# Kernel tuning notes

Hardware: AMD Instinct MI355X
Metric: run time of the kernel (lower is better)

The kernel has to match this reference:

```python
import jax, jax.numpy as jnp
import numpy as np

P, Q = 3, 3          # degrees
M, N = 127, 127      # max span index per direction (ctrl grid is (M+1)x(N+1))
DIM = 3
SU, SV = 256, 256    # out_dim_u, out_dim_v
B = 16
EPS = 1e-08


def _normalize_knots(knots):
    # cumsum of positive increments, rescaled to [0, 1]
    kc = jnp.cumsum(jnp.where(knots < 0.0, 0.0001, knots), axis=1)
    return (kc - kc[:, :1]) / (kc[:, -1:] - kc[:, :1])


def _find_spans(t, K, deg, max_span):
    # t: [S], K: [B, LK] -> spans [B, S] (first interior knot with t - K > EPS, else 1 sentinel)
    d = t[None, None, :] - K[:, deg:-deg, None]          # [B, L_int, S]
    masked = jnp.where(d > EPS, d, 1.0)
    return jnp.clip(jnp.argmin(masked, axis=1) + deg, deg, max_span)


def _basis(t, K, span, deg):
    # Cox-de Boor recursion. t: [S], K: [B, LK], span: [B, S] int -> [B, deg+1, S]
    Bsz, S = span.shape
    tb = t[None, :]
    Ni = [jnp.zeros((Bsz, S), K.dtype) for _ in range(deg + 1)]
    Ni[0] = jnp.ones((Bsz, S), K.dtype)
    for k in range(1, deg + 1):
        saved = jnp.zeros((Bsz, S), K.dtype)
        for r in range(k):
            K1 = jnp.take_along_axis(K, span + r + 1, axis=1)       # [B, S]
            K2 = jnp.take_along_axis(K, span + 1 - k + r, axis=1)   # [B, S]
            denom = (K1 - tb) + (tb - K2)
            temp = jnp.where(denom == 0.0, 0.0001,
                             Ni[r] / jnp.where(denom == 0.0, 1.0, denom))
            Ni[r] = saved + (K1 - tb) * temp
            saved = (tb - K2) * temp
        Ni[k] = saved
    return jnp.stack(Ni, axis=1)


def setup_inputs() -> dict:
    key = jax.random.key(0)
    k1, k2, k3 = jax.random.split(key, 3)
    ctrl_pts = jax.random.normal(k1, (B, M + 1, N + 1, DIM), dtype=jnp.float32)
    knot_u = jax.random.uniform(k2, (B, M + P + 2), dtype=jnp.float32)
    knot_v = jax.random.uniform(k3, (B, N + Q + 2), dtype=jnp.float32)
    u = jnp.linspace(1e-05, 1.0 - 1e-05, SU, dtype=jnp.float32)
    v = jnp.linspace(1e-05, 1.0 - 1e-05, SV, dtype=jnp.float32)
    return {"ctrl_pts": ctrl_pts, "knot_u": knot_u, "knot_v": knot_v, "u": u, "v": v}


def reference(ctrl_pts, knot_u, knot_v, u, v):
    U = _normalize_knots(knot_u)   # [B, M+P+2]
    V = _normalize_knots(knot_v)
    uspan = _find_spans(u, U, P, M)   # [B, SU] int
    vspan = _find_spans(v, V, Q, N)   # [B, SV] int
    Nu = _basis(u, U, uspan, P)       # [B, P+1, SU]
    Nv = _basis(v, V, vspan, Q)       # [B, Q+1, SV]
    # gather control points: pts[b,l,r,i,j,:] = ctrl_pts[b, uspan[b,i]-P+l, vspan[b,j]-Q+r, :]
    u_idx = uspan[:, None, :] - P + jnp.arange(P + 1)[None, :, None]  # [B, P+1, SU]
    v_idx = vspan[:, None, :] - Q + jnp.arange(Q + 1)[None, :, None]  # [B, Q+1, SV]
    b_idx = jnp.arange(B)[:, None, None, None, None]
    pts = ctrl_pts[b_idx,
                   u_idx[:, :, None, :, None],
                   v_idx[:, None, :, None, :], :]  # [B, P+1, Q+1, SU, SV, DIM]
    surfaces = jnp.einsum('bpquvd,bpu,bqv->buvd', pts, Nu, Nv)
    return surfaces[..., :DIM]
```

## Files before the change

kernel.cpp:

```cpp
#include <hip/hip_runtime.h>

#define BATCH 16
#define PDEG  3
#define MAXSPAN 127
#define KLEN  132
#define NSAMP 256
#define NSPANS 126
#define GRID_PTS 128
#define ROWF (GRID_PTS * 3)

__device__ __align__(16) float g_N[2][BATCH][NSAMP][4];
__device__ int   g_span[2][BATCH][NSAMP];

__global__ void basis_kernel(const float* __restrict__ knot_u,
                             const float* __restrict__ knot_v,
                             const float* __restrict__ u_arr,
                             const float* __restrict__ v_arr)
{
    __shared__ double sA[KLEN];
    __shared__ double sB[KLEN];
    const int b    = blockIdx.x;
    const int axis = blockIdx.y;
    const int tid  = threadIdx.x;

    const float* __restrict__ knots = axis ? knot_v : knot_u;
    const float* __restrict__ t_arr = axis ? v_arr  : u_arr;

    if (tid < KLEN) {
        float w = knots[b * KLEN + tid];
        sA[tid] = (w < 0.0f) ? 1.0e-4 : (double)w;
    }
    __syncthreads();

    double* src = sA;
    double* dst = sB;
    for (int off = 1; off < KLEN; off <<= 1) {
        if (tid < KLEN) {
            double v = src[tid];
            if (tid >= off) v += src[tid - off];
            dst[tid] = v;
        }
        __syncthreads();
        double* t_ = src; src = dst; dst = t_;
    }
    const double k0  = src[0];
    const double inv = 1.0 / (src[KLEN - 1] - k0);
    if (tid < KLEN) dst[tid] = (src[tid] - k0) * inv;
    __syncthreads();
    const double* __restrict__ kn = dst;

    const double t = (double)t_arr[tid];

    double best = 1.0e300;
    int jmin = 0;
    for (int j = 0; j < NSPANS; ++j) {
        double d = t - kn[j + PDEG];
        double m = (d > 1.0e-8) ? d : 1.0;
        if (m < best) { best = m; jmin = j; }
    }
    int span = jmin + PDEG;
    if (span > MAXSPAN) span = MAXSPAN;

    double Ni[PDEG + 1];
    Ni[0] = 1.0;
    for (int k = 1; k <= PDEG; ++k) {
        double saved = 0.0;
        for (int r = 0; r < k; ++r) {
            double K1 = kn[span + r + 1];
            double K2 = kn[span + 1 - k + r];
            double denom = (K1 - t) + (t - K2);
            double temp = (denom == 0.0) ? 1.0e-4 : (Ni[r] / denom);
            Ni[r] = saved + (K1 - t) * temp;
            saved = (t - K2) * temp;
        }
        Ni[k] = saved;
    }

    float4 o4;
    o4.x = (float)Ni[0]; o4.y = (float)Ni[1];
    o4.z = (float)Ni[2]; o4.w = (float)Ni[3];
    *(float4*)&g_N[axis][b][tid][0] = o4;
    g_span[axis][b][tid] = span;
}

__global__ void __launch_bounds__(256)
eval_kernel(const float* __restrict__ ctrl, float* __restrict__ out)
{
    __shared__ float s_tmp[ROWF];
    const int sv = threadIdx.x;
    const int su = blockIdx.x;
    const int b  = blockIdx.y;

    const int us = g_span[0][b][su];
    const float4 nu4 = *(const float4*)&g_N[0][b][su][0];

    const int vs = g_span[1][b][sv];
    const float4 nv4 = *(const float4*)&g_N[1][b][sv][0];
    const float nv[4] = {nv4.x, nv4.y, nv4.z, nv4.w};

    if (sv < ROWF / 4) {
        const float4* __restrict__ r0 = (const float4*)
            (ctrl + ((size_t)b * GRID_PTS + (size_t)(us - PDEG)) * ROWF);
        float4 a0 = r0[0 * 96 + sv];
        float4 a1 = r0[1 * 96 + sv];
        float4 a2 = r0[2 * 96 + sv];
        float4 a3 = r0[3 * 96 + sv];
        float4 t4;
        t4.x = nu4.x * a0.x + nu4.y * a1.x + nu4.z * a2.x + nu4.w * a3.x;
        t4.y = nu4.x * a0.y + nu4.y * a1.y + nu4.z * a2.y + nu4.w * a3.y;
        t4.z = nu4.x * a0.z + nu4.y * a1.z + nu4.z * a2.z + nu4.w * a3.z;
        t4.w = nu4.x * a0.w + nu4.y * a1.w + nu4.z * a2.w + nu4.w * a3.w;
        ((float4*)s_tmp)[sv] = t4;
    }

    __syncthreads();

    const float* tp = s_tmp + (vs - PDEG) * 3;
    float acc0 = 0.f, acc1 = 0.f, acc2 = 0.f;
#pragma unroll
    for (int q = 0; q < 4; ++q) {
        const float w = nv[q];
        acc0 += w * tp[q * 3 + 0];
        acc1 += w * tp[q * 3 + 1];
        acc2 += w * tp[q * 3 + 2];
    }

    const size_t o = (((size_t)b * NSAMP + su) * NSAMP + sv) * 3;
    out[o + 0] = acc0;
    out[o + 1] = acc1;
    out[o + 2] = acc2;
}

extern "C" void kernel_launch(void* const* d_in, const int* in_sizes, int n_in,
                              void* d_out, int out_size, void* d_ws, size_t ws_size,
                              hipStream_t stream) {
    const float* ctrl   = (const float*)d_in[0];
    const float* knot_u = (const float*)d_in[1];
    const float* knot_v = (const float*)d_in[2];
    const float* u      = (const float*)d_in[3];
    const float* v      = (const float*)d_in[4];
    float* out = (float*)d_out;

    dim3 bgrid(BATCH, 2);
    basis_kernel<<<bgrid, NSAMP, 0, stream>>>(knot_u, knot_v, u, v);

    dim3 egrid(NSAMP, BATCH);
    eval_kernel<<<egrid, NSAMP, 0, stream>>>(ctrl, out);
}
```

Measured before the change: 74.80 us.

## Fuse basis computation into surface evaluation kernel with per-block recompute

Merges the separate basis/span kernel into the evaluation kernel. Each block recomputes the normalized knots, the v basis for all samples and the u basis for its 16 rows in shared memory. It then processes 16 u-rows, two at a time, with double-buffered shared tmp rows. This removes a kernel launch and the global round-trip for basis data. In exchange the knot scan and span search are repeated redundantly per block, and the grid shrinks to 256 blocks, which may reduce parallelism.

```diff
diff --git a/kernel.cpp b/kernel.cpp
--- a/kernel.cpp
+++ b/kernel.cpp
@@ -8,49 +8,11 @@
 #define NSPANS 126
 #define GRID_PTS 128
 #define ROWF (GRID_PTS * 3)
+#define SU_PER_BLK 16
 
-__device__ __align__(16) float g_N[2][BATCH][NSAMP][4];
-__device__ int   g_span[2][BATCH][NSAMP];
-
-__global__ void basis_kernel(const float* __restrict__ knot_u,
-                             const float* __restrict__ knot_v,
-                             const float* __restrict__ u_arr,
-                             const float* __restrict__ v_arr)
+__device__ __forceinline__ int basis1(const double* __restrict__ kn,
+                                      double t, double Ni[PDEG + 1])
 {
-    __shared__ double sA[KLEN];
-    __shared__ double sB[KLEN];
-    const int b    = blockIdx.x;
-    const int axis = blockIdx.y;
-    const int tid  = threadIdx.x;
-
-    const float* __restrict__ knots = axis ? knot_v : knot_u;
-    const float* __restrict__ t_arr = axis ? v_arr  : u_arr;
-
-    if (tid < KLEN) {
-        float w = knots[b * KLEN + tid];
-        sA[tid] = (w < 0.0f) ? 1.0e-4 : (double)w;
-    }
-    __syncthreads();
-
-    double* src = sA;
-    double* dst = sB;
-    for (int off = 1; off < KLEN; off <<= 1) {
-        if (tid < KLEN) {
-            double v = src[tid];
-            if (tid >= off) v += src[tid - off];
-            dst[tid] = v;
-        }
-        __syncthreads();
-        double* t_ = src; src = dst; dst = t_;
-    }
-    const double k0  = src[0];
-    const double inv = 1.0 / (src[KLEN - 1] - k0);
-    if (tid < KLEN) dst[tid] = (src[tid] - k0) * inv;
-    __syncthreads();
-    const double* __restrict__ kn = dst;
-
-    const double t = (double)t_arr[tid];
-
     double best = 1.0e300;
     int jmin = 0;
     for (int j = 0; j < NSPANS; ++j) {
@@ -61,7 +23,6 @@
     int span = jmin + PDEG;
     if (span > MAXSPAN) span = MAXSPAN;
 
-    double Ni[PDEG + 1];
     Ni[0] = 1.0;
     for (int k = 1; k <= PDEG; ++k) {
         double saved = 0.0;
@@ -75,60 +36,133 @@
         }
         Ni[k] = saved;
     }
-
-    float4 o4;
-    o4.x = (float)Ni[0]; o4.y = (float)Ni[1];
-    o4.z = (float)Ni[2]; o4.w = (float)Ni[3];
-    *(float4*)&g_N[axis][b][tid][0] = o4;
-    g_span[axis][b][tid] = span;
+    return span;
 }
 
-__global__ void __launch_bounds__(256)
-eval_kernel(const float* __restrict__ ctrl, float* __restrict__ out)
+__global__ void __launch_bounds__(512)
+surf_kernel(const float* __restrict__ ctrl,
+            const float* __restrict__ knot_u,
+            const float* __restrict__ knot_v,
+            const float* __restrict__ u_arr,
+            const float* __restrict__ v_arr,
+            float* __restrict__ out)
 {
-    __shared__ float s_tmp[ROWF];
-    const int sv = threadIdx.x;
-    const int su = blockIdx.x;
-    const int b  = blockIdx.y;
+    __shared__ double sU[2][KLEN];
+    __shared__ double sV[2][KLEN];
+    __shared__ __align__(16) float sNv[NSAMP][4];
+    __shared__ int   sSv[NSAMP];
+    __shared__ __align__(16) float sNu[SU_PER_BLK][4];
+    __shared__ int   sSu[SU_PER_BLK];
+    __shared__ float s_tmp[2][2][ROWF];
 
-    const int us = g_span[0][b][su];
-    const float4 nu4 = *(const float4*)&g_N[0][b][su][0];
+    const int t   = threadIdx.x;
+    const int su0 = blockIdx.x * SU_PER_BLK;
+    const int b   = blockIdx.y;
 
-    const int vs = g_span[1][b][sv];
-    const float4 nv4 = *(const float4*)&g_N[1][b][sv][0];
-    const float nv[4] = {nv4.x, nv4.y, nv4.z, nv4.w};
-
-    if (sv < ROWF / 4) {
-        const float4* __restrict__ r0 = (const float4*)
-            (ctrl + ((size_t)b * GRID_PTS + (size_t)(us - PDEG)) * ROWF);
-        float4 a0 = r0[0 * 96 + sv];
-        float4 a1 = r0[1 * 96 + sv];
-        float4 a2 = r0[2 * 96 + sv];
-        float4 a3 = r0[3 * 96 + sv];
-        float4 t4;
-        t4.x = nu4.x * a0.x + nu4.y * a1.x + nu4.z * a2.x + nu4.w * a3.x;
-        t4.y = nu4.x * a0.y + nu4.y * a1.y + nu4.z * a2.y + nu4.w * a3.y;
-        t4.z = nu4.x * a0.z + nu4.y * a1.z + nu4.z * a2.z + nu4.w * a3.z;
-        t4.w = nu4.x * a0.w + nu4.y * a1.w + nu4.z * a2.w + nu4.w * a3.w;
-        ((float4*)s_tmp)[sv] = t4;
+    if (t < KLEN) {
+        float w = knot_u[b * KLEN + t];
+        sU[0][t] = (w < 0.0f) ? 1.0e-4 : (double)w;
+    } else if (t >= 256 && t < 256 + KLEN) {
+        const int i = t - 256;
+        float w = knot_v[b * KLEN + i];
+        sV[0][i] = (w < 0.0f) ? 1.0e-4 : (double)w;
     }
-
     __syncthreads();
 
-    const float* tp = s_tmp + (vs - PDEG) * 3;
-    float acc0 = 0.f, acc1 = 0.f, acc2 = 0.f;
+    int sb = 0;
+    for (int off = 1; off < KLEN; off <<= 1) {
+        if (t < KLEN) {
+            double v = sU[sb][t];
+            if (t >= off) v += sU[sb][t - off];
+            sU[sb ^ 1][t] = v;
+        } else if (t >= 256 && t < 256 + KLEN) {
+            const int i = t - 256;
+            double v = sV[sb][i];
+            if (i >= off) v += sV[sb][i - off];
+            sV[sb ^ 1][i] = v;
+        }
+        __syncthreads();
+        sb ^= 1;
+    }
+    if (t < KLEN) {
+        const double k0  = sU[sb][0];
+        const double inv = 1.0 / (sU[sb][KLEN - 1] - k0);
+        sU[sb ^ 1][t] = (sU[sb][t] - k0) * inv;
+    } else if (t >= 256 && t < 256 + KLEN) {
+        const int i = t - 256;
+        const double k0  = sV[sb][0];
+        const double inv = 1.0 / (sV[sb][KLEN - 1] - k0);
+        sV[sb ^ 1][i] = (sV[sb][i] - k0) * inv;
+    }
+    __syncthreads();
+    const double* __restrict__ knU = sU[sb ^ 1];
+    const double* __restrict__ knV = sV[sb ^ 1];
+
+    if (t < NSAMP) {
+        double Ni[PDEG + 1];
+        const int span = basis1(knV, (double)v_arr[t], Ni);
+        float4 o4;
+        o4.x = (float)Ni[0]; o4.y = (float)Ni[1];
+        o4.z = (float)Ni[2]; o4.w = (float)Ni[3];
+        *(float4*)&sNv[t][0] = o4;
+        sSv[t] = span;
+    } else if (t < NSAMP + SU_PER_BLK) {
+        const int j = t - NSAMP;
+        double Ni[PDEG + 1];
+        const int span = basis1(knU, (double)u_arr[su0 + j], Ni);
+        float4 o4;
+        o4.x = (float)Ni[0]; o4.y = (float)Ni[1];
+        o4.z = (float)Ni[2]; o4.w = (float)Ni[3];
+        *(float4*)&sNu[j][0] = o4;
+        sSu[j] = span;
+    }
+    __syncthreads();
+
+    const int r  = t >> 8;
+    const int sv = t & 255;
+    for (int i = 0; i < SU_PER_BLK / 2; ++i) {
+        const int buf = i & 1;
+        if (t < 192) {
+            const int pr = (t >= 96) ? 1 : 0;
+            const int c  = t - pr * 96;
+            const int sl = 2 * i + pr;
+            const int us = sSu[sl];
+            const float4 nu4 = *(const float4*)&sNu[sl][0];
+            const float4* __restrict__ r0 = (const float4*)
+                (ctrl + ((size_t)b * GRID_PTS + (size_t)(us - PDEG)) * ROWF);
+            float4 a0 = r0[0 * 96 + c];
+            float4 a1 = r0[1 * 96 + c];
+            float4 a2 = r0[2 * 96 + c];
+            float4 a3 = r0[3 * 96 + c];
+            float4 t4;
+            t4.x = nu4.x * a0.x + nu4.y * a1.x + nu4.z * a2.x + nu4.w * a3.x;
+            t4.y = nu4.x * a0.y + nu4.y * a1.y + nu4.z * a2.y + nu4.w * a3.y;
+            t4.z = nu4.x * a0.z + nu4.y * a1.z + nu4.z * a2.z + nu4.w * a3.z;
+            t4.w = nu4.x * a0.w + nu4.y * a1.w + nu4.z * a2.w + nu4.w * a3.w;
+            ((float4*)s_tmp[buf][pr])[c] = t4;
+        }
+        __syncthreads();
+        {
+            const int sl = 2 * i + r;
+            const int vs = sSv[sv];
+            const float4 nv4 = *(const float4*)&sNv[sv][0];
+            const float* tp = s_tmp[buf][r] + (vs - PDEG) * 3;
+            float acc0 = 0.f, acc1 = 0.f, acc2 = 0.f;
 #pragma unroll
-    for (int q = 0; q < 4; ++q) {
-        const float w = nv[q];
-        acc0 += w * tp[q * 3 + 0];
-        acc1 += w * tp[q * 3 + 1];
-        acc2 += w * tp[q * 3 + 2];
+            for (int q = 0; q < 4; ++q) {
+                const float w = (q == 0) ? nv4.x : (q == 1) ? nv4.y
+                              : (q == 2) ? nv4.z : nv4.w;
+                acc0 += w * tp[q * 3 + 0];
+                acc1 += w * tp[q * 3 + 1];
+                acc2 += w * tp[q * 3 + 2];
+            }
+            const size_t o = (((size_t)b * NSAMP + (size_t)(su0 + sl)) * NSAMP
+                              + (size_t)sv) * 3;
+            out[o + 0] = acc0;
+            out[o + 1] = acc1;
+            out[o + 2] = acc2;
+        }
     }
-
-    const size_t o = (((size_t)b * NSAMP + su) * NSAMP + sv) * 3;
-    out[o + 0] = acc0;
-    out[o + 1] = acc1;
-    out[o + 2] = acc2;
 }
 
 extern "C" void kernel_launch(void* const* d_in, const int* in_sizes, int n_in,
@@ -141,9 +175,6 @@
     const float* v      = (const float*)d_in[4];
     float* out = (float*)d_out;
 
-    dim3 bgrid(BATCH, 2);
-    basis_kernel<<<bgrid, NSAMP, 0, stream>>>(knot_u, knot_v, u, v);
-
-    dim3 egrid(NSAMP, BATCH);
-    eval_kernel<<<egrid, NSAMP, 0, stream>>>(ctrl, out);
+    dim3 grid(NSAMP / SU_PER_BLK, BATCH);
+    surf_kernel<<<grid, 512, 0, stream>>>(ctrl, knot_u, knot_v, u, v, out);
 }
```

After: 77.61 us. 1.04x slower.
